# Optimization experiments

Measured on AMD Instinct MI355X. Metric: run time of the kernel, lower is better.

The kernel has to match this reference:

```python
import jax, jax.numpy as jnp
import numpy as np

BLANK = 0          # tf.nn.ctc_loss default blank_index (StringLookup reserves 0 for OOV)
PAD = 127          # padding_value = char_to_num.vocabulary_size()
NEG = -1e30        # log-space 'zero' (avoid -inf to keep grads NaN-free)
B, T, C, L = 1024, 256, 128, 32


def setup_inputs() -> dict:
    key = jax.random.key(0)
    k1, k2 = jax.random.split(key)
    # labels in [1, PAD-1]; none equal PAD so label_length == L (full-length labels)
    y_true = jax.random.randint(k1, (B, L), 1, PAD).astype(jnp.int32)
    y_pred = jax.random.normal(k2, (B, T, C), dtype=jnp.float32)
    return {"y_true": y_true, "y_pred": y_pred}


def _ctc_loss(y_true, y_pred):
    """Faithful jax version of tf.nn.ctc_loss(labels, logits, label_len, T,
    logits_time_major=False, blank_index=0): standard log-space alpha DP."""
    Bn, Tn, Cn = y_pred.shape
    Ln = y_true.shape[1]
    S = 2 * Ln + 1  # extended label length (blanks interleaved)

    logp = jax.nn.log_softmax(y_pred, axis=-1)                    # [B,T,C]

    # extended label sequence: blank, l1, blank, l2, ..., blank   # [B,S]
    ext = jnp.full((Bn, S), BLANK, dtype=y_true.dtype)
    ext = ext.at[:, 1::2].set(y_true)

    # log-probs gathered at extended-label symbols                # [B,T,S]
    lp_ext = jnp.take_along_axis(
        logp, jnp.broadcast_to(ext[:, None, :], (Bn, Tn, S)), axis=2)

    # label_length = count of non-padding entries (mirrors count_nonzero)
    label_len = jnp.sum(y_true != PAD, axis=1)                    # [B]

    # skip transition s-2 -> s allowed iff ext[s] is a non-blank differing
    # from ext[s-2]
    skip_ok = jnp.concatenate(
        [jnp.zeros((Bn, 2), bool),
         (ext[:, 2:] != BLANK) & (ext[:, 2:] != ext[:, :-2])], axis=1)  # [B,S]

    neg1 = jnp.full((Bn, 1), NEG, logp.dtype)
    neg2 = jnp.full((Bn, 2), NEG, logp.dtype)

    alpha0 = jnp.full((Bn, S), NEG, logp.dtype)
    alpha0 = alpha0.at[:, 0].set(lp_ext[:, 0, 0]).at[:, 1].set(lp_ext[:, 0, 1])

    def step(alpha, lp_t):  # alpha,[B,S]  lp_t,[B,S]
        a1 = jnp.concatenate([neg1, alpha[:, :-1]], axis=1)
        a2 = jnp.concatenate([neg2, alpha[:, :-2]], axis=1)
        a2 = jnp.where(skip_ok, a2, NEG)
        new = lp_t + jnp.logaddexp(jnp.logaddexp(alpha, a1), a2)
        return new, None

    lp_seq = jnp.transpose(lp_ext, (1, 0, 2))                     # [T,B,S]
    alphaT, _ = jax.lax.scan(step, alpha0, lp_seq[1:])            # [B,S]

    # total log-likelihood ends at last blank (2*len) or last label (2*len-1)
    bi = jnp.arange(Bn)
    e1 = 2 * label_len
    e2 = 2 * label_len - 1
    loglik = jnp.logaddexp(alphaT[bi, e1], alphaT[bi, e2])        # [B]
    return -loglik


def reference(y_true, y_pred):
    # The original layer returns y_pred and registers the loss via add_loss;
    # the compute-dominant quantity is the per-example CTC loss, returned here.
    return _ctc_loss(y_true, y_pred)
```

## Files before the change

### kernel.cpp

```cpp
#include <hip/hip_runtime.h>
#include <cstdint>


#define CTC_BLANK 0
#define CTC_PAD   127
#define NEG       (-1e30f)
#define LOG2E     1.44269504088896340736f
#define LN2       0.69314718055994530942f

constexpr int Bn = 1024, Tn = 256, Cn = 128, Ln = 32;
constexpr int NSLOT = Ln + 1;
constexpr int PF = 4;

__device__ __forceinline__ float fexp2(float x) { return __builtin_amdgcn_exp2f(x); }
__device__ __forceinline__ float flog2(float x) { return __builtin_amdgcn_logf(x); }

template <int CTRL>
__device__ __forceinline__ float dpp_add(float s) {
    int v = __builtin_amdgcn_update_dpp(0, __float_as_int(s), CTRL, 0xF, 0xF, true);
    return s + __int_as_float(v);
}
__device__ __forceinline__ float dpp_wave_shr1(float src, float old) {
    return __int_as_float(__builtin_amdgcn_update_dpp(
        __float_as_int(old), __float_as_int(src), 0x138, 0xF, 0xF, false));
}

__global__ __launch_bounds__(256, 4) void ctc_fused_kernel(
        const int*   __restrict__ y_true,
        const float* __restrict__ y_pred,
        float*       __restrict__ out)
{
    __shared__ _Float16 Gc[Tn * NSLOT];
    __shared__ int   labels[Ln];
    __shared__ __align__(16) int cmap[Cn];
    __shared__ int   used[Cn];
    __shared__ int   wcnt[4];
    __shared__ float partS[8];

    const int b    = blockIdx.x;
    const int tid  = threadIdx.x;
    const int lane = tid & 63;
    const int wave = tid >> 6;

    if (tid < Ln) labels[tid] = y_true[b * Ln + tid];
    if (tid < Cn) used[tid] = 0;
    __syncthreads();
    if (tid == 0) used[CTC_BLANK] = 1;
    if (tid < Ln) used[labels[tid]] = 1;
    __syncthreads();
    {
        bool f = (tid < Cn) && (used[tid] != 0);
        unsigned long long m = __ballot(f);
        if (lane == 0) wcnt[wave] = __popcll(m);
        __syncthreads();
        int base = 0;
        for (int w = 0; w < wave; ++w) base += wcnt[w];
        if (tid < Cn)
            cmap[tid] = f ? (base + __popcll(m & ((1ull << lane) - 1ull))) : -1;
        __syncthreads();
    }

    const float* rowbase = y_pred + (size_t)b * Tn * Cn;
    const int half = lane >> 5;
    const int l32  = lane & 31;
    const int4 cm  = ((const int4*)cmap)[l32];
    float acc = 0.f;

    float4 v[2][8];
    #pragma unroll
    for (int j = 0; j < 8; ++j) {
        const int r = (wave * 4 + 0) * 16 + j * 2 + half;
        v[0][j] = ((const float4*)(rowbase + r * Cn))[l32];
    }
    for (int g = 0; g < 4; ++g) {
        if (g < 3) {
            #pragma unroll
            for (int j = 0; j < 8; ++j) {
                const int r = (wave * 4 + g + 1) * 16 + j * 2 + half;
                v[(g + 1) & 1][j] = ((const float4*)(rowbase + r * Cn))[l32];
            }
        }
        #pragma unroll
        for (int j = 0; j < 8; ++j) {
            const float4 x = v[g & 1][j];
            const int r = (wave * 4 + g) * 16 + j * 2 + half;
            if (cm.x >= 0) Gc[r * NSLOT + cm.x] = (_Float16)(x.x * LOG2E);
            if (cm.y >= 0) Gc[r * NSLOT + cm.y] = (_Float16)(x.y * LOG2E);
            if (cm.z >= 0) Gc[r * NSLOT + cm.z] = (_Float16)(x.z * LOG2E);
            if (cm.w >= 0) Gc[r * NSLOT + cm.w] = (_Float16)(x.w * LOG2E);
            float s = __expf(x.x) + __expf(x.y) + __expf(x.z) + __expf(x.w);
            s = dpp_add<0x111>(s);
            s = dpp_add<0x112>(s);
            s = dpp_add<0x114>(s);
            s = dpp_add<0x118>(s);
            s = dpp_add<0x142>(s);
            acc += __logf(s);
        }
    }
    if (l32 == 31) partS[wave * 2 + half] = acc;
    __syncthreads();

    if (wave == 0) {
        const int i = lane;
        const bool validO = (i < Ln);
        const bool validE = (i <= Ln);
        const int  myLab   = validO ? labels[i] : -1;
        const int  prevLab = (i >= 1 && i < Ln) ? labels[i - 1] : -1;
        const int  slotO   = validO ? cmap[myLab] : 0;
        const bool skipO   = (i >= 1 && i < Ln) &&
                             (myLab != CTC_BLANK) && (myLab != prevLab);
        const int  len = __popcll(__ballot(validO && (myLab != CTC_PAD)));

        float aE = (i == 0) ? (float)Gc[0]     : NEG;
        float aO = (i == 0) ? (float)Gc[slotO] : NEG;

        float pB[PF], pO[PF];
        #pragma unroll
        for (int j = 0; j < PF; ++j) {
            const int tj = 1 + j;
            pB[j] = (float)Gc[tj * NSLOT];
            pO[j] = (float)Gc[tj * NSLOT + slotO];
        }
        #pragma unroll 4
        for (int t = 1; t < Tn; ++t) {
            const float lpB = pB[0], lpO = pO[0];
            #pragma unroll
            for (int j = 0; j < PF - 1; ++j) { pB[j] = pB[j + 1]; pO[j] = pO[j + 1]; }
            const int tn = (t + PF < Tn) ? t + PF : Tn - 1;
            pB[PF - 1] = (float)Gc[tn * NSLOT];
            pO[PF - 1] = (float)Gc[tn * NSLOT + slotO];

            const float aOup = dpp_wave_shr1(aO, NEG);
            const float m  = fmaxf(aE, aOup);
            const float e1 = fexp2(aE - m);
            const float e2 = fexp2(aOup - m);
            const float sE = e1 + e2;
            const float nE = lpB + m + flog2(sE);
            const float m3 = fmaxf(aO, m);
            const float nO = lpO + m3 +
                flog2(fexp2(aO - m3) + (skipO ? sE : e1) * fexp2(m - m3));
            aE = validE ? nE : NEG;
            aO = validO ? nO : NEG;
        }

        const float v1 = __shfl(aE, len, 64);
        const float v2 = __shfl(aO, len - 1, 64);
        if (i == 0) {
            const float S = partS[0] + partS[1] + partS[2] + partS[3] +
                            partS[4] + partS[5] + partS[6] + partS[7];
            const float mm = fmaxf(v1, v2);
            const float L2 = mm + flog2(fexp2(v1 - mm) + fexp2(v2 - mm));
            out[b] = S - LN2 * L2;
        }
    }
}

extern "C" void kernel_launch(void* const* d_in, const int* in_sizes, int n_in,
                              void* d_out, int out_size, void* d_ws, size_t ws_size,
                              hipStream_t stream) {
    const int*   y_true = (const int*)d_in[0];
    const float* y_pred = (const float*)d_in[1];
    float*       out    = (float*)d_out;
    ctc_fused_kernel<<<Bn, 256, 0, stream>>>(y_true, y_pred, out);
}
```

Measured before the change: 220.2 us.

## Split time axis into chunks and overlap DP with loading of next chunk

Doubles the block to 512 threads and splits the time axis into two halves. Wave 0 runs the alpha recursion on the first half while the other waves load and convert the second half of the logits into shared memory, so the serial DP overlaps part of the global loads. The prefetch depth in the DP loop drops from four to two, and the block-wide barriers now include the DP wave. Larger blocks and an occupancy hint of 8 may cost registers or occupancy.

```diff
diff --git a/kernel.cpp b/kernel.cpp
--- a/kernel.cpp
+++ b/kernel.cpp
@@ -10,7 +10,8 @@
 
 constexpr int Bn = 1024, Tn = 256, Cn = 128, Ln = 32;
 constexpr int NSLOT = Ln + 1;
-constexpr int PF = 4;
+constexpr int NCH = 2;
+constexpr int CR  = Tn / NCH;
 
 __device__ __forceinline__ float fexp2(float x) { return __builtin_amdgcn_exp2f(x); }
 __device__ __forceinline__ float flog2(float x) { return __builtin_amdgcn_logf(x); }
@@ -25,7 +26,7 @@
         __float_as_int(old), __float_as_int(src), 0x138, 0xF, 0xF, false));
 }
 
-__global__ __launch_bounds__(256, 4) void ctc_fused_kernel(
+__global__ __launch_bounds__(512, 8) void ctc_fused_kernel(
         const int*   __restrict__ y_true,
         const float* __restrict__ y_pred,
         float*       __restrict__ out)
@@ -34,8 +35,8 @@
     __shared__ int   labels[Ln];
     __shared__ __align__(16) int cmap[Cn];
     __shared__ int   used[Cn];
-    __shared__ int   wcnt[4];
-    __shared__ float partS[8];
+    __shared__ int   wcnt[8];
+    __shared__ float partS[16];
 
     const int b    = blockIdx.x;
     const int tid  = threadIdx.x;
@@ -66,69 +67,36 @@
     const int4 cm  = ((const int4*)cmap)[l32];
     float acc = 0.f;
 
-    float4 v[2][8];
-    #pragma unroll
-    for (int j = 0; j < 8; ++j) {
-        const int r = (wave * 4 + 0) * 16 + j * 2 + half;
-        v[0][j] = ((const float4*)(rowbase + r * Cn))[l32];
-    }
-    for (int g = 0; g < 4; ++g) {
-        if (g < 3) {
-            #pragma unroll
-            for (int j = 0; j < 8; ++j) {
-                const int r = (wave * 4 + g + 1) * 16 + j * 2 + half;
-                v[(g + 1) & 1][j] = ((const float4*)(rowbase + r * Cn))[l32];
-            }
+    const int  i      = lane;
+    const bool validO = (i < Ln);
+    const bool validE = (i <= Ln);
+    const int  myLab   = validO ? labels[i] : -1;
+    const int  prevLab = (i >= 1 && i < Ln) ? labels[i - 1] : -1;
+    const int  slotO   = validO ? cmap[myLab] : 0;
+    const bool skipO   = (i >= 1 && i < Ln) &&
+                         (myLab != CTC_BLANK) && (myLab != prevLab);
+    const int  len = __popcll(__ballot(validO && (myLab != CTC_PAD)));
+    float aE = NEG, aO = NEG;
+
+    auto dp_chunk = [&](int t0, int t1) {
+        int t = t0;
+        if (t == 0) {
+            aE = (i == 0) ? (float)Gc[0]     : NEG;
+            aO = (i == 0) ? (float)Gc[slotO] : NEG;
+            t = 1;
         }
-        #pragma unroll
-        for (int j = 0; j < 8; ++j) {
-            const float4 x = v[g & 1][j];
-            const int r = (wave * 4 + g) * 16 + j * 2 + half;
-            if (cm.x >= 0) Gc[r * NSLOT + cm.x] = (_Float16)(x.x * LOG2E);
-            if (cm.y >= 0) Gc[r * NSLOT + cm.y] = (_Float16)(x.y * LOG2E);
-            if (cm.z >= 0) Gc[r * NSLOT + cm.z] = (_Float16)(x.z * LOG2E);
-            if (cm.w >= 0) Gc[r * NSLOT + cm.w] = (_Float16)(x.w * LOG2E);
-            float s = __expf(x.x) + __expf(x.y) + __expf(x.z) + __expf(x.w);
-            s = dpp_add<0x111>(s);
-            s = dpp_add<0x112>(s);
-            s = dpp_add<0x114>(s);
-            s = dpp_add<0x118>(s);
-            s = dpp_add<0x142>(s);
-            acc += __logf(s);
-        }
-    }
-    if (l32 == 31) partS[wave * 2 + half] = acc;
-    __syncthreads();
-
-    if (wave == 0) {
-        const int i = lane;
-        const bool validO = (i < Ln);
-        const bool validE = (i <= Ln);
-        const int  myLab   = validO ? labels[i] : -1;
-        const int  prevLab = (i >= 1 && i < Ln) ? labels[i - 1] : -1;
-        const int  slotO   = validO ? cmap[myLab] : 0;
-        const bool skipO   = (i >= 1 && i < Ln) &&
-                             (myLab != CTC_BLANK) && (myLab != prevLab);
-        const int  len = __popcll(__ballot(validO && (myLab != CTC_PAD)));
-
-        float aE = (i == 0) ? (float)Gc[0]     : NEG;
-        float aO = (i == 0) ? (float)Gc[slotO] : NEG;
-
-        float pB[PF], pO[PF];
-        #pragma unroll
-        for (int j = 0; j < PF; ++j) {
-            const int tj = 1 + j;
-            pB[j] = (float)Gc[tj * NSLOT];
-            pO[j] = (float)Gc[tj * NSLOT + slotO];
-        }
-        #pragma unroll 4
-        for (int t = 1; t < Tn; ++t) {
-            const float lpB = pB[0], lpO = pO[0];
-            #pragma unroll
-            for (int j = 0; j < PF - 1; ++j) { pB[j] = pB[j + 1]; pO[j] = pO[j + 1]; }
-            const int tn = (t + PF < Tn) ? t + PF : Tn - 1;
-            pB[PF - 1] = (float)Gc[tn * NSLOT];
-            pO[PF - 1] = (float)Gc[tn * NSLOT + slotO];
+        float pB[2], pO[2];
+        const int ta = t, tb = (t + 1 < t1) ? t + 1 : t1 - 1;
+        pB[0] = (float)Gc[ta * NSLOT]; pO[0] = (float)Gc[ta * NSLOT + slotO];
+        pB[1] = (float)Gc[tb * NSLOT]; pO[1] = (float)Gc[tb * NSLOT + slotO];
+        int k = 0;
+        #pragma unroll 2
+        for (; t < t1; ++t) {
+            const float lpB = pB[k], lpO = pO[k];
+            const int tp = (t + 2 < t1) ? t + 2 : t1 - 1;
+            pB[k] = (float)Gc[tp * NSLOT];
+            pO[k] = (float)Gc[tp * NSLOT + slotO];
+            k ^= 1;
 
             const float aOup = dpp_wave_shr1(aO, NEG);
             const float m  = fmaxf(aE, aOup);
@@ -142,12 +110,46 @@
             aE = validE ? nE : NEG;
             aO = validO ? nO : NEG;
         }
+    };
 
+    for (int c = 0; c < NCH; ++c) {
+        if (wave == 0 && c > 0) dp_chunk((c - 1) * CR, c * CR);
+
+        const int cbase = c * CR;
+        float4 v[8];
+        #pragma unroll
+        for (int j = 0; j < 8; ++j) {
+            const int r = cbase + 2 * (wave * 8 + j) + half;
+            v[j] = ((const float4*)(rowbase + r * Cn))[l32];
+        }
+        #pragma unroll
+        for (int j = 0; j < 8; ++j) {
+            const int r = cbase + 2 * (wave * 8 + j) + half;
+            const float4 x = v[j];
+            if (cm.x >= 0) Gc[r * NSLOT + cm.x] = (_Float16)(x.x * LOG2E);
+            if (cm.y >= 0) Gc[r * NSLOT + cm.y] = (_Float16)(x.y * LOG2E);
+            if (cm.z >= 0) Gc[r * NSLOT + cm.z] = (_Float16)(x.z * LOG2E);
+            if (cm.w >= 0) Gc[r * NSLOT + cm.w] = (_Float16)(x.w * LOG2E);
+            float s = __expf(x.x) + __expf(x.y) + __expf(x.z) + __expf(x.w);
+            s = dpp_add<0x111>(s);
+            s = dpp_add<0x112>(s);
+            s = dpp_add<0x114>(s);
+            s = dpp_add<0x118>(s);
+            s = dpp_add<0x142>(s);
+            acc += __logf(s);
+        }
+        if (c == NCH - 1 && l32 == 31) partS[wave * 2 + half] = acc;
+        __syncthreads();
+    }
+
+    if (wave == 0) {
+        dp_chunk((NCH - 1) * CR, Tn);
         const float v1 = __shfl(aE, len, 64);
         const float v2 = __shfl(aO, len - 1, 64);
         if (i == 0) {
-            const float S = partS[0] + partS[1] + partS[2] + partS[3] +
-                            partS[4] + partS[5] + partS[6] + partS[7];
+            float S = 0.f;
+            #pragma unroll
+            for (int j = 0; j < 16; ++j) S += partS[j];
             const float mm = fmaxf(v1, v2);
             const float L2 = mm + flog2(fexp2(v1 - mm) + fexp2(v2 - mm));
             out[b] = S - LN2 * L2;
@@ -161,5 +163,5 @@
     const int*   y_true = (const int*)d_in[0];
     const float* y_pred = (const float*)d_in[1];
     float*       out    = (float*)d_out;
-    ctc_fused_kernel<<<Bn, 256, 0, stream>>>(y_true, y_pred, out);
+    ctc_fused_kernel<<<Bn, 512, 0, stream>>>(y_true, y_pred, out);
 }
```

Result: faster. 209.3 us (-5.0%).
